# Kernel optimization log

Hardware: AMD Instinct MI355X
Metric: run time of the kernel (lower is better)

The kernel has to match this reference:

```python
import jax, jax.numpy as jnp
import numpy as np

BS, N_STK, N_STK_PNT = 4, 32, 128
N_PNT = N_STK * N_STK_PNT
SP_IN, DN_IN = 128, 128
SP_OUT, DN_OUT = 256, 256
SP_NEAR, DN_NEAR = 2, 10
COOR = 128


def _conv2d(x, w, b, stride=(1, 1), pad='VALID'):
    # x [bs,C,H,W], w [O,I,kh,kw]
    y = jax.lax.conv_general_dilated(x, w, window_strides=stride, padding=pad,
                                     dimension_numbers=('NCHW', 'OIHW', 'NCHW'))
    return y + b[None, :, None, None]


def _fps(xyz, n_sample):
    # farthest point sampling. xyz [bs,n,c] -> [bs,n_sample] int32
    n = xyz.shape[1]

    def one(x):
        def body(i, state):
            idx, dist, far = state
            idx = idx.at[i].set(far)
            d = jnp.sum((x - x[far]) ** 2, axis=-1)
            dist = jnp.minimum(dist, d)
            return idx, dist, jnp.argmax(dist).astype(jnp.int32)

        idx0 = jnp.zeros((n_sample,), jnp.int32)
        dist0 = jnp.full((n,), 1e10, x.dtype)
        idx, _, _ = jax.lax.fori_loop(0, n_sample, body, (idx0, dist0, jnp.int32(0)))
        return idx

    return jax.vmap(one)(xyz)


def _gcn(x, W, b, g, bt, k):
    # DGCNN edge-conv. x [bs,c,n]; W [2c,co]
    xt = jnp.swapaxes(x, 1, 2)                                   # [bs,n,c]
    sq = jnp.sum(xt * xt, axis=-1)                               # [bs,n]
    dist = sq[:, :, None] - 2.0 * jnp.einsum('bnc,bmc->bnm', xt, xt) + sq[:, None, :]
    _, idx = jax.lax.top_k(-dist, k)                             # [bs,n,k]
    nbr = jax.vmap(lambda p, i: p[i])(xt, idx)                   # [bs,n,k,c]
    ctr = jnp.broadcast_to(xt[:, :, None, :], nbr.shape)
    edge = jnp.concatenate([ctr, nbr - ctr], axis=-1)            # [bs,n,k,2c]
    h = jnp.einsum('bnke,eo->bnko', edge, W) + b
    h = jax.nn.relu(g * h + bt)
    return jnp.swapaxes(jnp.max(h, axis=2), 1, 2)                # [bs,co,n]


def setup_inputs() -> dict:
    key = jax.random.key(0)
    ks = jax.random.split(key, 16)
    f32 = jnp.float32
    d = {
        'sparse_fea': jax.random.normal(ks[0], (BS, SP_IN, N_STK), f32),
        'dense_fea': jax.random.normal(ks[1], (BS, DN_IN, N_PNT), f32),
        'stk_coor': jax.random.normal(ks[2], (BS, N_STK, COOR), f32),
        # DenseToSparse: Conv2d(dn_in->dn_in, (1,3)) + BN
        'd2s_w': jax.random.normal(ks[3], (DN_IN, DN_IN, 1, 3), f32) * 0.05,
        'd2s_b': jnp.zeros((DN_IN,), f32),
        'd2s_g': jnp.ones((DN_IN,), f32),
        'd2s_bt': jnp.zeros((DN_IN,), f32),
        # sparse GCN: in = SP_IN + DN_IN, edge feat 2*in
        'sp_W': jax.random.normal(ks[4], (2 * (SP_IN + DN_IN), SP_OUT), f32) * 0.05,
        'sp_b': jnp.zeros((SP_OUT,), f32),
        'sp_g': jnp.ones((SP_OUT,), f32),
        'sp_bt': jnp.zeros((SP_OUT,), f32),
        # dense GCN: in = DN_IN + SP_IN
        'dn_W': jax.random.normal(ks[5], (2 * (DN_IN + SP_IN), DN_OUT), f32) * 0.05,
        'dn_b': jnp.zeros((DN_OUT,), f32),
        'dn_g': jnp.ones((DN_OUT,), f32),
        'dn_bt': jnp.zeros((DN_OUT,), f32),
        # DownSample: Conv2d(dn_out->dn_out, (1,3), stride (1,2), pad (0,1)) + BN
        'ds_w': jax.random.normal(ks[6], (DN_OUT, DN_OUT, 1, 3), f32) * 0.05,
        'ds_b': jnp.zeros((DN_OUT,), f32),
        'ds_g': jnp.ones((DN_OUT,), f32),
        'ds_bt': jnp.zeros((DN_OUT,), f32),
    }
    return d


def reference(sparse_fea, dense_fea, stk_coor,
              d2s_w, d2s_b, d2s_g, d2s_bt,
              sp_W, sp_b, sp_g, sp_bt,
              dn_W, dn_b, dn_g, dn_bt,
              ds_w, ds_b, ds_g, ds_bt):
    bs = sparse_fea.shape[0]
    df = dense_fea.reshape(bs, DN_IN, N_STK, N_STK_PNT)
    # DenseToSparse: conv (1,3) valid + BN(eval) + relu + max over stroke points
    h = _conv2d(df, d2s_w, d2s_b)
    h = jax.nn.relu(d2s_g[None, :, None, None] * h + d2s_bt[None, :, None, None])
    sp_from_dn = jnp.max(h, axis=3)                                    # [bs,dn_in,n_stk]
    union_sparse = jnp.concatenate([sparse_fea, sp_from_dn], axis=1)   # [bs,sp_in+dn_in,n_stk]
    # SparseToDense: broadcast stroke feature onto its points
    dn_from_sp = jnp.broadcast_to(sparse_fea[:, :, :, None], (bs, SP_IN, N_STK, N_STK_PNT))
    union_dense = jnp.concatenate([df, dn_from_sp], axis=1).reshape(bs, DN_IN + SP_IN, N_PNT)
    # GCN (DGCNN edge conv) updates
    sparse_up = _gcn(union_sparse, sp_W, sp_b, sp_g, sp_bt, SP_NEAR)   # [bs,SP_OUT,n_stk]
    dense_up = _gcn(union_dense, dn_W, dn_b, dn_g, dn_bt, DN_NEAR)     # [bs,DN_OUT,n_pnt]
    # DownSample: FPS on stroke coords, gather strokes, strided conv on points
    n_half = N_STK // 2
    fps_idx = _fps(stk_coor, n_half)                                   # [bs,n_half]
    stk_coor_s = jnp.take_along_axis(stk_coor, fps_idx[:, :, None], axis=1)
    sp_s = jnp.take_along_axis(jnp.swapaxes(sparse_up, 1, 2), fps_idx[:, :, None], axis=1)
    sp_s = jnp.swapaxes(sp_s, 1, 2)                                    # [bs,SP_OUT,n_half]
    dn = dense_up.reshape(bs, DN_OUT, N_STK, N_STK_PNT)
    dn = jnp.take_along_axis(dn, fps_idx[:, None, :, None], axis=2)    # [bs,DN_OUT,n_half,n_stk_pnt]
    dn = _conv2d(dn, ds_w, ds_b, stride=(1, 2), pad=[(0, 0), (1, 1)])
    dn = jax.nn.relu(ds_g[None, :, None, None] * dn + ds_bt[None, :, None, None])
    dn = dn.reshape(bs, DN_OUT, n_half * (N_STK_PNT // 2))
    return sp_s, dn, stk_coor_s
```

## Files before the change

### kernel.cpp

```cpp
#include <hip/hip_runtime.h>

#define NPNT 4096
#define NSTK 32

typedef _Float16 half8 __attribute__((ext_vector_type(8)));
typedef float f32x4 __attribute__((ext_vector_type(4)));
typedef unsigned long long u64;

static const size_t OFF_XT   = 0;
static const size_t OFF_P    = 4194304;
static const size_t OFF_Q    = 8388608;
static const size_t OFF_SQD  = 12582912;
static const size_t OFF_SPFD = 12599296;
static const size_t OFF_XS   = 12615680;
static const size_t OFF_PS   = 12648448;
static const size_t OFF_QS   = 12681216;
static const size_t OFF_WSP  = 12746752;
static const size_t OFF_KNN  = 13402112;
static const size_t OFF_IDXS = 13565952;
static const size_t OFF_FPS  = 13566208;
static const size_t OFF_SD   = 13566272;

__device__ __forceinline__ void insertK(u64 lk[10], u64 k) {
  if (k >= lk[9]) return;
  lk[9] = k;
#pragma unroll
  for (int j = 9; j > 0; j--) {
    u64 a = lk[j-1], b2 = lk[j];
    bool sw = b2 < a;
    lk[j-1] = sw ? b2 : a;
    lk[j]   = sw ? a : b2;
  }
}

#define CASK(a, b) { u64 _x = (a), _y = (b); bool _s = _y < _x; \
  (a) = _s ? _y : _x; (b) = _s ? _x : _y; }

__device__ __forceinline__ void merge10(u64 lk[10], const u64 b[10]) {
  u64 c[10];
#pragma unroll
  for (int i = 0; i < 10; i++) { u64 t = b[9 - i]; u64 a = lk[i]; c[i] = a < t ? a : t; }
  CASK(c[0], c[5]); CASK(c[1], c[6]); CASK(c[2], c[7]); CASK(c[3], c[8]); CASK(c[4], c[9]);
  CASK(c[0], c[1]); CASK(c[1], c[2]); CASK(c[2], c[3]); CASK(c[3], c[4]);
  CASK(c[0], c[1]); CASK(c[1], c[2]); CASK(c[2], c[3]);
  CASK(c[0], c[1]); CASK(c[1], c[2]);
  CASK(c[0], c[1]);
  CASK(c[5], c[6]); CASK(c[6], c[7]); CASK(c[7], c[8]); CASK(c[8], c[9]);
  CASK(c[5], c[6]); CASK(c[6], c[7]); CASK(c[7], c[8]);
  CASK(c[5], c[6]); CASK(c[6], c[7]);
  CASK(c[5], c[6]);
#pragma unroll
  for (int i = 0; i < 10; i++) lk[i] = c[i];
}

__global__ __launch_bounds__(256) void k_pre(
    const float* __restrict__ df, const float* __restrict__ sf,
    const float* __restrict__ coor, const float* __restrict__ dnW,
    const float* __restrict__ d2sw, const float* __restrict__ d2scb,
    const float* __restrict__ d2sg, const float* __restrict__ d2sbt,
    const float* __restrict__ dsw,
    _Float16* __restrict__ XH, _Float16* __restrict__ XL, float* __restrict__ sqd,
    _Float16* __restrict__ WPh, _Float16* __restrict__ WPl,
    _Float16* __restrict__ WQh, _Float16* __restrict__ WQl,
    float* __restrict__ WDP,
    float* __restrict__ spfd, int* __restrict__ fpsidx, float* __restrict__ out2) {
  __shared__ __align__(16) char SMEM[46080];
  const int bid = blockIdx.x;
  const int t = threadIdx.x;

  if (bid < 4) {
    int b = bid;
    float (*X)[132] = (float (*)[132])SMEM;
    float* dist = (float*)(SMEM + 16896);
    int* far_s  = (int*)(SMEM + 17024);
    int* sel    = (int*)(SMEM + 17028);
    for (int idx = t; idx < 32 * 32; idx += 256) {
      int r = idx >> 5, q = idx & 31;
      *(float4*)&X[r][q * 4] = *(const float4*)&coor[((size_t)b * 32 + r) * 128 + q * 4];
    }
    if (t < 32) dist[t] = 1e10f;
    if (t == 0) *far_s = 0;
    __syncthreads();
    for (int it = 0; it < 16; it++) {
      int far = *far_s;
      if (t == 0) sel[it] = far;
      if (t < 32) {
        float d = 0.0f;
        for (int c = 0; c < 128; c++) { float dd = X[t][c] - X[far][c]; d = fmaf(dd, dd, d); }
        float dm = dist[t];
        dist[t] = d < dm ? d : dm;
      }
      __syncthreads();
      if (t == 0) {
        float best = -1.0f; int bi = 0;
        for (int m = 0; m < 32; m++) if (dist[m] > best) { best = dist[m]; bi = m; }
        *far_s = bi;
      }
      __syncthreads();
    }
    if (t < 16) fpsidx[b * 16 + t] = sel[t];
    __syncthreads();
    for (int idx = t; idx < 16 * 32; idx += 256) {
      int j = idx >> 5, q = idx & 31;
      *(float4*)&out2[((size_t)b * 16 + j) * 128 + q * 4] = *(const float4*)&X[sel[j]][q * 4];
    }
  } else if (bid < 260) {
    int idx0 = bid - 4;
    int b = idx0 & 3, n0 = (idx0 >> 2) * 64;
    int s0 = n0 >> 7;
    float (*T)[68] = (float (*)[68])SMEM;
    _Float16* Sh = (_Float16*)(SMEM + 34816);
    _Float16* Sl = (_Float16*)(SMEM + 35072);
    {
      int c = t >> 1, nh = (t & 1) * 32;
      const float* src = &df[((size_t)b * 128 + c) * NPNT + n0 + nh];
#pragma unroll
      for (int j = 0; j < 8; j++) *(float4*)&T[c][nh + j * 4] = *(const float4*)&src[j * 4];
    }
    if (t < 128) {
      float x = sf[((size_t)b * 128 + t) * NSTK + s0];
      _Float16 hi = (_Float16)x;
      Sh[t] = hi; Sl[t] = (_Float16)(x - (float)hi);
    }
    __syncthreads();
    {
      int n = t >> 2, cseg = (t & 3) * 32;
      size_t base = ((size_t)b * NPNT + n0 + n) * 256;
      float s = 0.0f;
#pragma unroll
      for (int k = 0; k < 4; k++) {
        half8 hv, lv, shv, slv;
#pragma unroll
        for (int e = 0; e < 8; e++) {
          float x = T[cseg + k * 8 + e][n];
          s = fmaf(x, x, s);
          _Float16 hi = (_Float16)x;
          hv[e] = hi; lv[e] = (_Float16)(x - (float)hi);
          shv[e] = Sh[cseg + k * 8 + e];
          slv[e] = Sl[cseg + k * 8 + e];
        }
        *(half8*)&XH[base + cseg + k * 8] = hv;
        *(half8*)&XL[base + cseg + k * 8] = lv;
        *(half8*)&XH[base + 128 + cseg + k * 8] = shv;
        *(half8*)&XL[base + 128 + cseg + k * 8] = slv;
      }
      s += __shfl_xor(s, 1);
      s += __shfl_xor(s, 2);
      if ((t & 3) == 0) sqd[(size_t)b * NPNT + n0 + n] = s;
    }
  } else if (bid < 516) {
    int idx0 = bid - 260;
    int b = idx0 & 3, o0 = ((idx0 >> 2) & 1) * 64, s = idx0 >> 3;
    int n0 = s * 128;
    float (*A)[64]   = (float (*)[64])SMEM;
    float (*Bs)[132] = (float (*)[132])(SMEM + 24576);
    float (*Dr)[17]  = (float (*)[17])(SMEM + 41472);
    float acc[4][8];
#pragma unroll
    for (int i = 0; i < 4; i++)
#pragma unroll
      for (int j = 0; j < 8; j++) acc[i][j] = 0.0f;
    int tn = t & 15, to = t >> 4;
    for (int ic = 0; ic < 128; ic += 32) {
      {
        int ol = t >> 2, q = t & 3;
        const float* src = &d2sw[((size_t)(o0 + ol) * 128 + ic) * 3 + q * 24];
#pragma unroll
        for (int r = 0; r < 6; r++) {
          float4 v = *(const float4*)&src[r * 4];
          int e = q * 24 + r * 4;
          A[e+0][ol] = v.x; A[e+1][ol] = v.y; A[e+2][ol] = v.z; A[e+3][ol] = v.w;
        }
      }
      for (int idx = t; idx < 32 * 33; idx += 256) {
        int row = idx / 33, f4 = idx % 33;
        int nb = n0 + f4 * 4;
        const float* srow = &df[((size_t)b * 128 + ic + row) * NPNT];
        float4 v;
        if (nb + 3 < NPNT) v = *(const float4*)&srow[nb];
        else {
          v.x = srow[nb   < NPNT ? nb   : NPNT-1];
          v.y = srow[nb+1 < NPNT ? nb+1 : NPNT-1];
          v.z = srow[nb+2 < NPNT ? nb+2 : NPNT-1];
          v.w = srow[nb+3 < NPNT ? nb+3 : NPNT-1];
// ... 15 lines not shown
            float bvj = bv[kw + j];
            acc[0][j] = fmaf(av.x, bvj, acc[0][j]);
            acc[1][j] = fmaf(av.y, bvj, acc[1][j]);
            acc[2][j] = fmaf(av.z, bvj, acc[2][j]);
            acc[3][j] = fmaf(av.w, bvj, acc[3][j]);
          }
        }
      }
      __syncthreads();
    }
#pragma unroll
    for (int i = 0; i < 4; i++) {
      int o = o0 + to * 4 + i;
      float gg = d2sg[o], bb = d2scb[o], bo = d2sbt[o];
      float m = 0.0f;
#pragma unroll
      for (int j = 0; j < 8; j++) {
        int p = tn * 8 + j;
        if (p < 126) {
          float v = fmaf(gg, acc[i][j] + bb, bo);
          v = v > 0.0f ? v : 0.0f;
          m = v > m ? v : m;
        }
      }
      Dr[to * 4 + i][tn] = m;
    }
    __syncthreads();
    if (t < 64) {
      float m = 0.0f;
#pragma unroll
      for (int k = 0; k < 16; k++) m = Dr[t][k] > m ? Dr[t][k] : m;
      spfd[((size_t)b * 128 + o0 + t) * NSTK + s] = m;
    }
  } else if (bid < 772) {
    int k = bid - 516, o = t;
    float w1 = dnW[(size_t)k * 256 + o];
    float w2 = dnW[(size_t)(k + 256) * 256 + o];
    float p = w1 - w2;
    _Float16 ph = (_Float16)p;  WPh[(size_t)o * 256 + k] = ph;
    WPl[(size_t)o * 256 + k] = (_Float16)(p - (float)ph);
    _Float16 qh = (_Float16)w2; WQh[(size_t)o * 256 + k] = qh;
    WQl[(size_t)o * 256 + k] = (_Float16)(w2 - (float)qh);
  } else {
    int o = bid - 772;
    const float* src = &dsw[(size_t)o * 768];
    float* dst = &WDP[(size_t)o * 768];
#pragma unroll
    for (int kw = 0; kw < 3; kw++)
      dst[kw * 256 + t] = src[t * 3 + kw];
  }
}

__global__ __launch_bounds__(256) void k_sparse_graph(const float* __restrict__ sf, const float* __restrict__ spfd,
    float* __restrict__ xs, int* __restrict__ idxs, float* __restrict__ SD) {
  int b = blockIdx.x, t = threadIdx.x;
  __shared__ float X[32][260];
  __shared__ float sq[32];
  __shared__ float D[32][33];
  for (int idx = t; idx < 32 * 256; idx += 256) {
    int n = idx >> 8, c = idx & 255;
    float v = (c < 128) ? sf[((size_t)b * 128 + c) * NSTK + n]
                        : spfd[((size_t)b * 128 + (c - 128)) * NSTK + n];
    X[n][c] = v;
  }
  __syncthreads();
  for (int idx = t; idx < 32 * 64; idx += 256) {
    int n = idx >> 6, q = idx & 63;
    *(float4*)&xs[((size_t)b * 32 + n) * 256 + q * 4] = *(const float4*)&X[n][q * 4];
  }
#pragma unroll
  for (int rep = 0; rep < 4; rep++) {
    int p = t + rep * 256;
    int s = p >> 5, u = p & 31;
    float acc = 0.0f;
    for (int c = 0; c < 128; c++) {
      float d = X[s][c] - X[u][c];
      acc = fmaf(d, d, acc);
    }
    SD[(size_t)b * 1024 + p] = acc;
  }
  if (t < 32) {
    float s = 0.0f;
    for (int c = 0; c < 256; c++) s = fmaf(X[t][c], X[t][c], s);
    sq[t] = s;
  }
  __syncthreads();
  {
    int n = t >> 3;
    for (int mg = 0; mg < 4; mg++) {
      int m = (t & 7) + mg * 8;
      float dot = 0.0f;
      for (int c = 0; c < 256; c++) dot = fmaf(X[n][c], X[m][c], dot);
      D[n][m] = (sq[n] - 2.0f * dot) + sq[m];
    }
  }
  __syncthreads();
  if (t < 32) {
    float d0 = 1e30f, d1 = 1e30f; int i0 = 0, i1 = 0;
    for (int m = 0; m < 32; m++) {
      float d = D[t][m];
      if (d < d0) { d1 = d0; i1 = i0; d0 = d; i0 = m; }
      else if (d < d1) { d1 = d; i1 = m; }
    }
    idxs[(b * 32 + t) * 2 + 0] = i0;
    idxs[(b * 32 + t) * 2 + 1] = i1;
  }
}

__global__ __launch_bounds__(256) void k_sparse_pq(const float* __restrict__ xs, const float* __restrict__ W,
    float* __restrict__ Ps, float* __restrict__ Qs) {
  int b = blockIdx.x >> 5, n = blockIdx.x & 31;
  int o = threadIdx.x;
  const float* xr = &xs[((size_t)b * 32 + n) * 256];
  float accP = 0.0f, accQ = 0.0f;
  for (int c = 0; c < 256; c++) {
    float xc = xr[c];
    float w1 = W[(size_t)c * 256 + o];
    float w2 = W[(size_t)(c + 256) * 256 + o];
    accP = fmaf(xc, w1 - w2, accP);
    accQ = fmaf(xc, w2, accQ);
  }
  Ps[((size_t)b * 32 + n) * 256 + o] = accP;
  Qs[((size_t)b * 32 + n) * 256 + o] = accQ;
}

__global__ __launch_bounds__(256) void k_sparse_cg(const float* __restrict__ Ps, const float* __restrict__ Qs,
    const int* __restrict__ idxs, const int* __restrict__ fps,
    const float* __restrict__ g, const float* __restrict__ cb, const float* __restrict__ bt,
    float* __restrict__ out0) {
  int b = blockIdx.x, j = blockIdx.y, o = threadIdx.x;
  int n = fps[b * 16 + j];
  int i0 = idxs[(b * 32 + n) * 2 + 0], i1 = idxs[(b * 32 + n) * 2 + 1];
  float p = Ps[((size_t)b * 32 + n) * 256 + o];
  float q0 = Qs[((size_t)b * 32 + i0) * 256 + o];
  float q1 = Qs[((size_t)b * 32 + i1) * 256 + o];
  float gg = g[o], bb = cb[o], bo = bt[o];
  float h0 = fmaf(gg, p + q0 + bb, bo); h0 = h0 > 0.0f ? h0 : 0.0f;
  float h1 = fmaf(gg, p + q1 + bb, bo); h1 = h1 > 0.0f ? h1 : 0.0f;
  out0[((size_t)b * 256 + o) * 16 + j] = h0 > h1 ? h0 : h1;
}

#define STAGE(ch2_, p_) { \
  int srow = t >> 2, scol = (t & 3) * 16; \
  size_t gp = (bofs + (size_t)(m0 + (ch2_) * 64 + srow)) * 256 + (p_) * 64 + scol; \
  float4 gh0 = *(const float4*)&XH[gp]; float4 gh1 = *(const float4*)&XH[gp + 8]; \
  float4 gl0 = *(const float4*)&XL[gp]; float4 gl1 = *(const float4*)&XL[gp + 8]; \
  int lo = srow * 72 + scol; \
  *(float4*)&BshH[lo] = gh0; *(float4*)&BshH[lo + 8] = gh1; \
  *(float4*)&BshL[lo] = gl0; *(float4*)&BshL[lo + 8] = gl1; }

#define DWU(wv_, r_, c_) DwU[(((wv_) * 16 + (r_)) * 68) + (c_)]

__global__ __launch_bounds__(256, 4) void k_knn_mfma(const _Float16* __restrict__ XH,
    const _Float16* __restrict__ XL, const float* __restrict__ sqd, const float* __restrict__ SD,
    const int* __restrict__ fps, u64* __restrict__ pk) {
  const int h = blockIdx.x, rb = blockIdx.y, b = blockIdx.z;
  const int t = threadIdx.x;
  const int w = t >> 6, L = t & 63;
  const int c15 = L & 15, q = L >> 4;
  const int jst = rb >> 1;
  const int ph = (rb & 1) * 64;
  const int s_stk = fps[b * 16 + jst];
  const int nsrc = s_stk * 128 + ph + w * 16;
  const int rc0 = rb * 64 + w * 16;
  const size_t bofs = (size_t)b * NPNT;

  __shared__ __align__(16) char SMEM[18432];
  _Float16* const BshH = (_Float16*)SMEM;
  _Float16* const BshL = (_Float16*)(SMEM + 64 * 72 * 2);
  unsigned* const DwU = (unsigned*)SMEM;

  half8 ah[4], al[4];
  {
    const _Float16* ap  = XH + (bofs + nsrc + c15) * 256 + q * 8;
    const _Float16* apl = XL + (bofs + nsrc + c15) * 256 + q * 8;
#pragma unroll
    for (int ch = 0; ch < 4; ch++) {
      ah[ch] = *(const half8*)(ap + ch * 32);
      al[ch] = *(const half8*)(apl + ch * 32);
    }
  }
  float snr[4];
#pragma unroll
  for (int r = 0; r < 4; r++) snr[r] = sqd[bofs + nsrc + q * 4 + r];

  u64 lk[10];
#pragma unroll
  for (int j = 0; j < 10; j++) lk[j] = ~0ull;
// ... 54 lines not shown

#pragma unroll
      for (int cg = 0; cg < 4; cg++) {
        float basec = SDv + smv[cg];
#pragma unroll
        for (int r = 0; r < 4; r++) {
          float d = fmaf(-2.0f, acc[cg][r], snr[r] + basec);
          unsigned uu = __float_as_uint(d);
          unsigned kk = uu ^ ((unsigned)((int)uu >> 31) | 0x80000000u);
          DWU(w, q * 4 + r, cg * 16 + c15) = kk;
        }
      }
#pragma unroll
      for (int jj = 0; jj < 4; jj++) {
        uint4 kv = *(const uint4*)&DWU(w, r_sel, jj * 16 + sl * 4);
        int ib = m0 + ch2 * 64 + jj * 16 + sl * 4;
        insertK(lk, ((u64)kv.x << 32) | (unsigned)(ib + 0));
        insertK(lk, ((u64)kv.y << 32) | (unsigned)(ib + 1));
        insertK(lk, ((u64)kv.z << 32) | (unsigned)(ib + 2));
        insertK(lk, ((u64)kv.w << 32) | (unsigned)(ib + 3));
      }
    }
  }

#pragma unroll
  for (int m = 1; m <= 2; m <<= 1) {
    u64 o[10];
#pragma unroll
    for (int j = 0; j < 10; j++) o[j] = __shfl_xor(lk[j], m);
    merge10(lk, o);
  }
  if (sl == 0) {
    size_t row = (size_t)b * 2048 + rc0 + r_sel;
    u64* dst = &pk[(row * 16 + h) * 10];
#pragma unroll
    for (int j = 0; j < 10; j++) dst[j] = lk[j];
  }
}

__global__ __launch_bounds__(256) void k_knn_merge(const u64* __restrict__ pk,
                                                   int* __restrict__ knnc) {
  int gid = blockIdx.x * 256 + threadIdx.x;
  size_t row = (size_t)(gid >> 2);
  int sl = gid & 3;
  const u64* src = &pk[row * 160 + (size_t)sl * 40];
  u64 lk[10];
#pragma unroll
  for (int j = 0; j < 10; j++) lk[j] = src[j];
#pragma unroll
  for (int l = 1; l < 4; l++) {
    u64 bv[10];
#pragma unroll
    for (int j = 0; j < 10; j++) bv[j] = src[l * 10 + j];
    merge10(lk, bv);
  }
#pragma unroll
  for (int m = 1; m <= 2; m <<= 1) {
    u64 o[10];
#pragma unroll
    for (int j = 0; j < 10; j++) o[j] = __shfl_xor(lk[j], m);
    merge10(lk, o);
  }
  if (sl == 0) {
#pragma unroll
    for (int j = 0; j < 10; j++) knnc[row * 10 + j] = (int)(unsigned)(lk[j] & 0xffffffffull);
  }
}

__global__ __launch_bounds__(256, 4) void k_pq_mfma(const _Float16* __restrict__ XH, const _Float16* __restrict__ XL,
    const _Float16* __restrict__ WPh, const _Float16* __restrict__ WPl,
    const _Float16* __restrict__ WQh, const _Float16* __restrict__ WQl,
    const int* __restrict__ fps, const float* __restrict__ g, const float* __restrict__ cb,
    const float* __restrict__ bt, float* __restrict__ Pc, float* __restrict__ Qp) {
  const int b = blockIdx.z;
  const int t = threadIdx.x, w = t >> 6, L = t & 63;
  const int c15 = L & 15, q = L >> 4;
  const int ow = blockIdx.y * 128 + (w >> 1) * 64;
  const size_t bofs = (size_t)b * NPNT;
  f32x4 zz = {0.0f, 0.0f, 0.0f, 0.0f};

  {
    const int nw = blockIdx.x * 32 + (w & 1) * 16;
    f32x4 accQ[4];
#pragma unroll
    for (int cg = 0; cg < 4; cg++) accQ[cg] = zz;
    const _Float16* ap  = XH + (bofs + nw + c15) * 256 + q * 8;
    const _Float16* apl = XL + (bofs + nw + c15) * 256 + q * 8;
#pragma unroll
    for (int ch = 0; ch < 8; ch++) {
      half8 a_h = *(const half8*)(ap + ch * 32);
      half8 a_l = *(const half8*)(apl + ch * 32);
#pragma unroll
      for (int cg = 0; cg < 4; cg++) {
        size_t wb = (size_t)(ow + cg * 16 + c15) * 256 + ch * 32 + q * 8;
        half8 bqh = *(const half8*)(WQh + wb);
        half8 bql = *(const half8*)(WQl + wb);
        accQ[cg] = __builtin_amdgcn_mfma_f32_16x16x32_f16(a_h, bqh, accQ[cg], 0, 0, 0);
        accQ[cg] = __builtin_amdgcn_mfma_f32_16x16x32_f16(a_h, bql, accQ[cg], 0, 0, 0);
        accQ[cg] = __builtin_amdgcn_mfma_f32_16x16x32_f16(a_l, bqh, accQ[cg], 0, 0, 0);
      }
    }
#pragma unroll
// ... 11 lines not shown
    const int m0 = blockIdx.x * 32 + (w & 1) * 16;
    const int jst = m0 >> 7;
    const int pbase = m0 & 127;
    const int nsrc = fps[b * 16 + jst] * 128 + pbase;
    f32x4 accP[4];
#pragma unroll
    for (int cg = 0; cg < 4; cg++) accP[cg] = zz;
    const _Float16* ap  = XH + (bofs + nsrc + c15) * 256 + q * 8;
    const _Float16* apl = XL + (bofs + nsrc + c15) * 256 + q * 8;
#pragma unroll
    for (int ch = 0; ch < 8; ch++) {
      half8 a_h = *(const half8*)(ap + ch * 32);
      half8 a_l = *(const half8*)(apl + ch * 32);
#pragma unroll
      for (int cg = 0; cg < 4; cg++) {
        size_t wb = (size_t)(ow + cg * 16 + c15) * 256 + ch * 32 + q * 8;
        half8 bph = *(const half8*)(WPh + wb);
        half8 bpl = *(const half8*)(WPl + wb);
        accP[cg] = __builtin_amdgcn_mfma_f32_16x16x32_f16(a_h, bph, accP[cg], 0, 0, 0);
        accP[cg] = __builtin_amdgcn_mfma_f32_16x16x32_f16(a_h, bpl, accP[cg], 0, 0, 0);
        accP[cg] = __builtin_amdgcn_mfma_f32_16x16x32_f16(a_l, bph, accP[cg], 0, 0, 0);
      }
    }
#pragma unroll
    for (int cg = 0; cg < 4; cg++) {
      int o = ow + cg * 16 + c15;
      float gg = g[o], bb = cb[o], bo = bt[o];
#pragma unroll
      for (int r = 0; r < 4; r++) {
        Pc[(((size_t)b * 16 + jst) * 128 + pbase + q * 4 + r) * 256 + o] =
            fmaf(gg, accP[cg][r] + bb, bo);
      }
    }
  }
}

__global__ __launch_bounds__(256) void k_build_M(const float* __restrict__ Pc, const float* __restrict__ Qp,
    const int* __restrict__ knnc, float* __restrict__ M) {
  int pc = blockIdx.x, j = blockIdx.y, b = blockIdx.z;
  int t = threadIdx.x;
  int p0 = pc * 16;
#pragma unroll 1
  for (int pi = 0; pi < 16; pi++) {
    size_t m = ((size_t)b * 16 + j) * 128 + p0 + pi;
    float pv = Pc[m * 256 + t];
    const int* id = &knnc[m * 10];
    float mx = 0.0f;
#pragma unroll
    for (int k = 0; k < 10; k++) {
      float qv = Qp[((size_t)b * NPNT + id[k]) * 256 + t];
      float h = pv + qv;
      mx = h > mx ? h : mx;
    }
    M[m * 256 + t] = mx;
  }
}

__global__ __launch_bounds__(256) void k_ds_gemm(const float* __restrict__ WDP, const float* __restrict__ M,
    const float* __restrict__ cb, const float* __restrict__ g, const float* __restrict__ bt,
    float* __restrict__ out1) {
  int j = blockIdx.x, o0 = blockIdx.y * 64, b = blockIdx.z;
  int j0 = j * 64;
  int t = threadIdx.x;
  __shared__ float A[32][68];
  __shared__ float Bs[32][68];
  float acc[4][4];
#pragma unroll
  for (int i = 0; i < 4; i++)
#pragma unroll
    for (int jj = 0; jj < 4; jj++) acc[i][jj] = 0.0f;
  int tj = t & 15, to = t >> 4;
  for (int kc = 0; kc < 768; kc += 32) {
    {
      int ol = t >> 2, q = t & 3;
      const float* src = &WDP[(size_t)(o0 + ol) * 768 + kc + q * 8];
      float4 v0 = *(const float4*)src, v1 = *(const float4*)(src + 4);
      int cc = q * 8;
      A[cc+0][ol] = v0.x; A[cc+1][ol] = v0.y; A[cc+2][ol] = v0.z; A[cc+3][ol] = v0.w;
      A[cc+4][ol] = v1.x; A[cc+5][ol] = v1.y; A[cc+6][ol] = v1.z; A[cc+7][ol] = v1.w;
    }
    {
      int jl = t >> 2, q = t & 3;
      int kw = kc >> 8, cbl = (kc & 255) + q * 8;
      int p = 2 * jl - 1 + kw;
      float4 v0, v1;
      if (p >= 0) {
        const float* src = &M[(((size_t)b * 16 + j) * 128 + p) * 256 + cbl];
// ... 32 lines not shown
    *(float4*)&out1[((size_t)b * 256 + o) * 1024 + j0 + tj * 4] = v;
  }
}

extern "C" void kernel_launch(void* const* d_in, const int* in_sizes, int n_in,
                              void* d_out, int out_size, void* d_ws, size_t ws_size,
                              hipStream_t stream) {
  (void)in_sizes; (void)n_in; (void)out_size; (void)ws_size;
  const float* sf    = (const float*)d_in[0];
  const float* df    = (const float*)d_in[1];
  const float* coor  = (const float*)d_in[2];
  const float* d2sw  = (const float*)d_in[3];
  const float* d2sb  = (const float*)d_in[4];
  const float* d2sg  = (const float*)d_in[5];
  const float* d2sbt = (const float*)d_in[6];
  const float* spW   = (const float*)d_in[7];
  const float* spb   = (const float*)d_in[8];
  const float* spg   = (const float*)d_in[9];
  const float* spbt  = (const float*)d_in[10];
  const float* dnW   = (const float*)d_in[11];
  const float* dnb   = (const float*)d_in[12];
  const float* dng   = (const float*)d_in[13];
  const float* dnbt  = (const float*)d_in[14];
  const float* dsw   = (const float*)d_in[15];
  const float* dsb   = (const float*)d_in[16];
  const float* dsg   = (const float*)d_in[17];
  const float* dsbt  = (const float*)d_in[18];

  float* ws   = (float*)d_ws;
  float* Pc   = ws + OFF_P;
  float* Qp   = ws + OFF_Q;
  float* SQD  = ws + OFF_SQD;
  float* SPFD = ws + OFF_SPFD;
  float* XS   = ws + OFF_XS;
  float* PS   = ws + OFF_PS;
  float* QS   = ws + OFF_QS;
  int*   KNNC = (int*)(ws + OFF_KNN);
  int*   IDXS = (int*)(ws + OFF_IDXS);
  int*   FPS  = (int*)(ws + OFF_FPS);
  float* SD   = ws + OFF_SD;
  _Float16* XT2H = (_Float16*)(ws + OFF_XT);
  _Float16* XT2L = XT2H + (size_t)4 * NPNT * 256;
  float* Mb = ws + OFF_XT;
  _Float16* WPh = (_Float16*)(ws + OFF_WSP);
  _Float16* WPl = WPh + 65536;
  _Float16* WQh = WPh + 131072;
  _Float16* WQl = WPh + 196608;
  float* WDP = ws + OFF_WSP + 131072;
  u64* PK = (u64*)(ws + OFF_Q);

  float* out0 = (float*)d_out;
  float* out1 = out0 + 16384;
  float* out2 = out1 + 1048576;

  k_pre<<<dim3(1028), 256, 0, stream>>>(df, sf, coor, dnW, d2sw, d2sb, d2sg, d2sbt, dsw,
                                        XT2H, XT2L, SQD, WPh, WPl, WQh, WQl, WDP,
                                        SPFD, FPS, out2);
  k_sparse_graph<<<dim3(4), 256, 0, stream>>>(sf, SPFD, XS, IDXS, SD);
  k_sparse_pq<<<dim3(128), 256, 0, stream>>>(XS, spW, PS, QS);
  k_sparse_cg<<<dim3(4, 16), 256, 0, stream>>>(PS, QS, IDXS, FPS, spg, spb, spbt, out0);
  k_knn_mfma<<<dim3(16, 32, 4), 256, 0, stream>>>(XT2H, XT2L, SQD, SD, FPS, PK);
  k_knn_merge<<<dim3(128), 256, 0, stream>>>(PK, KNNC);
  k_pq_mfma<<<dim3(128, 2, 4), 256, 0, stream>>>(XT2H, XT2L, WPh, WPl, WQh, WQl,
                                                 FPS, dng, dnb, dnbt, Pc, Qp);
  k_build_M<<<dim3(8, 16, 4), 256, 0, stream>>>(Pc, Qp, KNNC, Mb);
  k_ds_gemm<<<dim3(16, 4, 4), 256, 0, stream>>>(WDP, Mb, dsb, dsg, dsbt, out1);
}
```

Baseline: 417.2 us.

## Fuse sparse GCN kernels, merge kNN reduction into build_M, compact candidate storage

The three sparse-branch kernels become one single-block-per-batch kernel that computes neighbours, the Q projection into shared memory and P only for the FPS-selected strokes. The stroke distance matrix SD moves into extra k_pre blocks. The separate kNN merge kernel is removed: k_knn_mfma writes candidates as split 32-bit keys and 16-bit indices, and k_build_M merges the 16 partial lists with shuffles before gathering. Launch order and k_pq_mfma occupancy bounds also change. This cuts launches and intermediate global traffic, but the sparse kernel runs on only 4 blocks and does its GEMMs serially.

```diff
diff --git a/kernel.cpp b/kernel.cpp
--- a/kernel.cpp
+++ b/kernel.cpp
@@ -6,18 +6,15 @@
 typedef _Float16 half8 __attribute__((ext_vector_type(8)));
 typedef float f32x4 __attribute__((ext_vector_type(4)));
 typedef unsigned long long u64;
+typedef unsigned int u32;
+typedef unsigned short u16;
 
 static const size_t OFF_XT   = 0;
 static const size_t OFF_P    = 4194304;
 static const size_t OFF_Q    = 8388608;
 static const size_t OFF_SQD  = 12582912;
 static const size_t OFF_SPFD = 12599296;
-static const size_t OFF_XS   = 12615680;
-static const size_t OFF_PS   = 12648448;
-static const size_t OFF_QS   = 12681216;
 static const size_t OFF_WSP  = 12746752;
-static const size_t OFF_KNN  = 13402112;
-static const size_t OFF_IDXS = 13565952;
 static const size_t OFF_FPS  = 13566208;
 static const size_t OFF_SD   = 13566272;
 
@@ -62,7 +59,7 @@
     _Float16* __restrict__ XH, _Float16* __restrict__ XL, float* __restrict__ sqd,
     _Float16* __restrict__ WPh, _Float16* __restrict__ WPl,
     _Float16* __restrict__ WQh, _Float16* __restrict__ WQl,
-    float* __restrict__ WDP,
+    float* __restrict__ WDP, float* __restrict__ SD,
     float* __restrict__ spfd, int* __restrict__ fpsidx, float* __restrict__ out2) {
   __shared__ __align__(16) char SMEM[46080];
   const int bid = blockIdx.x;
@@ -104,8 +101,25 @@
       int j = idx >> 5, q = idx & 31;
       *(float4*)&out2[((size_t)b * 16 + j) * 128 + q * 4] = *(const float4*)&X[sel[j]][q * 4];
     }
-  } else if (bid < 260) {
-    int idx0 = bid - 4;
+  } else if (bid < 8) {
+    int b = bid - 4;
+    float* Xs = (float*)SMEM;
+    for (int k = t; k < 1024; k += 256)
+      *(float4*)&Xs[k * 4] = *(const float4*)&sf[(size_t)b * 4096 + k * 4];
+    __syncthreads();
+#pragma unroll
+    for (int rep = 0; rep < 4; rep++) {
+      int p = t + rep * 256;
+      int s = p >> 5, u = p & 31;
+      float acc = 0.0f;
+      for (int c = 0; c < 128; c++) {
+        float d = Xs[c * 32 + s] - Xs[c * 32 + u];
+        acc = fmaf(d, d, acc);
+      }
+      SD[(size_t)b * 1024 + p] = acc;
+    }
+  } else if (bid < 264) {
+    int idx0 = bid - 8;
     int b = idx0 & 3, n0 = (idx0 >> 2) * 64;
     int s0 = n0 >> 7;
     float (*T)[68] = (float (*)[68])SMEM;
@@ -148,8 +162,8 @@
       s += __shfl_xor(s, 2);
       if ((t & 3) == 0) sqd[(size_t)b * NPNT + n0 + n] = s;
     }
-  } else if (bid < 516) {
-    int idx0 = bid - 260;
+  } else if (bid < 520) {
+    int idx0 = bid - 264;
     int b = idx0 & 3, o0 = ((idx0 >> 2) & 1) * 64, s = idx0 >> 3;
     int n0 = s * 128;
     float (*A)[64]   = (float (*)[64])SMEM;
@@ -231,8 +245,8 @@
       for (int k = 0; k < 16; k++) m = Dr[t][k] > m ? Dr[t][k] : m;
       spfd[((size_t)b * 128 + o0 + t) * NSTK + s] = m;
     }
-  } else if (bid < 772) {
-    int k = bid - 516, o = t;
+  } else if (bid < 776) {
+    int k = bid - 520, o = t;
     float w1 = dnW[(size_t)k * 256 + o];
     float w2 = dnW[(size_t)(k + 256) * 256 + o];
     float p = w1 - w2;
@@ -241,7 +255,7 @@
     _Float16 qh = (_Float16)w2; WQh[(size_t)o * 256 + k] = qh;
     WQl[(size_t)o * 256 + k] = (_Float16)(w2 - (float)qh);
   } else {
-    int o = bid - 772;
+    int o = bid - 776;
     const float* src = &dsw[(size_t)o * 768];
     float* dst = &WDP[(size_t)o * 768];
 #pragma unroll
@@ -250,34 +264,25 @@
   }
 }
 
-__global__ __launch_bounds__(256) void k_sparse_graph(const float* __restrict__ sf, const float* __restrict__ spfd,
-    float* __restrict__ xs, int* __restrict__ idxs, float* __restrict__ SD) {
+__global__ __launch_bounds__(256) void k_sparse_mono(const float* __restrict__ sf,
+    const float* __restrict__ spfd, const int* __restrict__ fps, const float* __restrict__ W,
+    const float* __restrict__ g, const float* __restrict__ cb, const float* __restrict__ bt,
+    float* __restrict__ out0) {
   int b = blockIdx.x, t = threadIdx.x;
   __shared__ float X[32][260];
+  __shared__ float Qs[32][256];
+  __shared__ float D[32][33];
   __shared__ float sq[32];
-  __shared__ float D[32][33];
+  __shared__ int idxs_s[64];
+  __shared__ int fps_s[16];
   for (int idx = t; idx < 32 * 256; idx += 256) {
     int n = idx >> 8, c = idx & 255;
     float v = (c < 128) ? sf[((size_t)b * 128 + c) * NSTK + n]
                         : spfd[((size_t)b * 128 + (c - 128)) * NSTK + n];
     X[n][c] = v;
   }
+  if (t < 16) fps_s[t] = fps[b * 16 + t];
   __syncthreads();
-  for (int idx = t; idx < 32 * 64; idx += 256) {
-    int n = idx >> 6, q = idx & 63;
-    *(float4*)&xs[((size_t)b * 32 + n) * 256 + q * 4] = *(const float4*)&X[n][q * 4];
-  }
-#pragma unroll
-  for (int rep = 0; rep < 4; rep++) {
-    int p = t + rep * 256;
-    int s = p >> 5, u = p & 31;
-    float acc = 0.0f;
-    for (int c = 0; c < 128; c++) {
-      float d = X[s][c] - X[u][c];
-      acc = fmaf(d, d, acc);
-    }
-    SD[(size_t)b * 1024 + p] = acc;
-  }
   if (t < 32) {
     float s = 0.0f;
     for (int c = 0; c < 256; c++) s = fmaf(X[t][c], X[t][c], s);
@@ -301,42 +306,75 @@
       if (d < d0) { d1 = d0; i1 = i0; d0 = d; i0 = m; }
       else if (d < d1) { d1 = d; i1 = m; }
     }
-    idxs[(b * 32 + t) * 2 + 0] = i0;
-    idxs[(b * 32 + t) * 2 + 1] = i1;
-  }
-}
-
-__global__ __launch_bounds__(256) void k_sparse_pq(const float* __restrict__ xs, const float* __restrict__ W,
-    float* __restrict__ Ps, float* __restrict__ Qs) {
-  int b = blockIdx.x >> 5, n = blockIdx.x & 31;
-  int o = threadIdx.x;
-  const float* xr = &xs[((size_t)b * 32 + n) * 256];
-  float accP = 0.0f, accQ = 0.0f;
-  for (int c = 0; c < 256; c++) {
-    float xc = xr[c];
-    float w1 = W[(size_t)c * 256 + o];
-    float w2 = W[(size_t)(c + 256) * 256 + o];
-    accP = fmaf(xc, w1 - w2, accP);
-    accQ = fmaf(xc, w2, accQ);
-  }
-  Ps[((size_t)b * 32 + n) * 256 + o] = accP;
-  Qs[((size_t)b * 32 + n) * 256 + o] = accQ;
-}
-
-__global__ __launch_bounds__(256) void k_sparse_cg(const float* __restrict__ Ps, const float* __restrict__ Qs,
-    const int* __restrict__ idxs, const int* __restrict__ fps,
-    const float* __restrict__ g, const float* __restrict__ cb, const float* __restrict__ bt,
-    float* __restrict__ out0) {
-  int b = blockIdx.x, j = blockIdx.y, o = threadIdx.x;
-  int n = fps[b * 16 + j];
-  int i0 = idxs[(b * 32 + n) * 2 + 0], i1 = idxs[(b * 32 + n) * 2 + 1];
-  float p = Ps[((size_t)b * 32 + n) * 256 + o];
-  float q0 = Qs[((size_t)b * 32 + i0) * 256 + o];
-  float q1 = Qs[((size_t)b * 32 + i1) * 256 + o];
+    idxs_s[t * 2 + 0] = i0;
+    idxs_s[t * 2 + 1] = i1;
+  }
+  const int o = t;
+#pragma unroll 1
+  for (int nc = 0; nc < 4; nc++) {
+    float acc[8];
+#pragma unroll
+    for (int nn = 0; nn < 8; nn++) acc[nn] = 0.0f;
+    for (int c4 = 0; c4 < 64; c4++) {
+      float4 xv[8];
+#pragma unroll
+      for (int nn = 0; nn < 8; nn++) xv[nn] = *(const float4*)&X[nc * 8 + nn][c4 * 4];
+      int c = c4 * 4;
+      float w0 = W[(size_t)(c + 256) * 256 + o];
+      float w1 = W[(size_t)(c + 257) * 256 + o];
+      float w2 = W[(size_t)(c + 258) * 256 + o];
+      float w3 = W[(size_t)(c + 259) * 256 + o];
+#pragma unroll
+      for (int nn = 0; nn < 8; nn++) {
+        acc[nn] = fmaf(xv[nn].x, w0, acc[nn]);
+        acc[nn] = fmaf(xv[nn].y, w1, acc[nn]);
+        acc[nn] = fmaf(xv[nn].z, w2, acc[nn]);
+        acc[nn] = fmaf(xv[nn].w, w3, acc[nn]);
+      }
+    }
+#pragma unroll
+    for (int nn = 0; nn < 8; nn++) Qs[nc * 8 + nn][o] = acc[nn];
+  }
+  float pacc[16];
+#pragma unroll 1
+  for (int jc = 0; jc < 2; jc++) {
+    int fs[8];
+#pragma unroll
+    for (int jj = 0; jj < 8; jj++) fs[jj] = fps_s[jc * 8 + jj];
+    float acc[8];
+#pragma unroll
+    for (int jj = 0; jj < 8; jj++) acc[jj] = 0.0f;
+    for (int c4 = 0; c4 < 64; c4++) {
+      float4 xv[8];
+#pragma unroll
+      for (int jj = 0; jj < 8; jj++) xv[jj] = *(const float4*)&X[fs[jj]][c4 * 4];
+      int c = c4 * 4;
+      float p0 = W[(size_t)(c + 0) * 256 + o] - W[(size_t)(c + 256) * 256 + o];
+      float p1 = W[(size_t)(c + 1) * 256 + o] - W[(size_t)(c + 257) * 256 + o];
+      float p2 = W[(size_t)(c + 2) * 256 + o] - W[(size_t)(c + 258) * 256 + o];
+      float p3 = W[(size_t)(c + 3) * 256 + o] - W[(size_t)(c + 259) * 256 + o];
+#pragma unroll
+      for (int jj = 0; jj < 8; jj++) {
+        acc[jj] = fmaf(xv[jj].x, p0, acc[jj]);
+        acc[jj] = fmaf(xv[jj].y, p1, acc[jj]);
+        acc[jj] = fmaf(xv[jj].z, p2, acc[jj]);
+        acc[jj] = fmaf(xv[jj].w, p3, acc[jj]);
+      }
+    }
+#pragma unroll
+    for (int jj = 0; jj < 8; jj++) pacc[jc * 8 + jj] = acc[jj];
+  }
+  __syncthreads();
   float gg = g[o], bb = cb[o], bo = bt[o];
-  float h0 = fmaf(gg, p + q0 + bb, bo); h0 = h0 > 0.0f ? h0 : 0.0f;
-  float h1 = fmaf(gg, p + q1 + bb, bo); h1 = h1 > 0.0f ? h1 : 0.0f;
-  out0[((size_t)b * 256 + o) * 16 + j] = h0 > h1 ? h0 : h1;
+#pragma unroll
+  for (int j = 0; j < 16; j++) {
+    int n = fps_s[j];
+    int i0 = idxs_s[n * 2 + 0], i1 = idxs_s[n * 2 + 1];
+    float p = pacc[j];
+    float h0 = fmaf(gg, p + Qs[i0][o] + bb, bo); h0 = h0 > 0.0f ? h0 : 0.0f;
+    float h1 = fmaf(gg, p + Qs[i1][o] + bb, bo); h1 = h1 > 0.0f ? h1 : 0.0f;
+    out0[((size_t)b * 256 + o) * 16 + j] = h0 > h1 ? h0 : h1;
+  }
 }
 
 #define STAGE(ch2_, p_) { \
@@ -352,7 +390,7 @@
 
 __global__ __launch_bounds__(256, 4) void k_knn_mfma(const _Float16* __restrict__ XH,
     const _Float16* __restrict__ XL, const float* __restrict__ sqd, const float* __restrict__ SD,
-    const int* __restrict__ fps, u64* __restrict__ pk) {
+    const int* __restrict__ fps, u32* __restrict__ pkd, u16* __restrict__ pki) {
   const int h = blockIdx.x, rb = blockIdx.y, b = blockIdx.z;
   const int t = threadIdx.x;
   const int w = t >> 6, L = t & 63;
@@ -473,42 +511,58 @@
   }
   if (sl == 0) {
     size_t row = (size_t)b * 2048 + rc0 + r_sel;
-    u64* dst = &pk[(row * 16 + h) * 10];
-#pragma unroll
-    for (int j = 0; j < 10; j++) dst[j] = lk[j];
-  }
-}
-
-__global__ __launch_bounds__(256) void k_knn_merge(const u64* __restrict__ pk,
-                                                   int* __restrict__ knnc) {
-  int gid = blockIdx.x * 256 + threadIdx.x;
-  size_t row = (size_t)(gid >> 2);
-  int sl = gid & 3;
-  const u64* src = &pk[row * 160 + (size_t)sl * 40];
-  u64 lk[10];
-#pragma unroll
-  for (int j = 0; j < 10; j++) lk[j] = src[j];
-#pragma unroll
-  for (int l = 1; l < 4; l++) {
-    u64 bv[10];
-#pragma unroll
-    for (int j = 0; j < 10; j++) bv[j] = src[l * 10 + j];
-    merge10(lk, bv);
-  }
-#pragma unroll
-  for (int m = 1; m <= 2; m <<= 1) {
-    u64 o[10];
-#pragma unroll
-    for (int j = 0; j < 10; j++) o[j] = __shfl_xor(lk[j], m);
-    merge10(lk, o);
-  }
-  if (sl == 0) {
-#pragma unroll
-    for (int j = 0; j < 10; j++) knnc[row * 10 + j] = (int)(unsigned)(lk[j] & 0xffffffffull);
-  }
-}
-
-__global__ __launch_bounds__(256, 4) void k_pq_mfma(const _Float16* __restrict__ XH, const _Float16* __restrict__ XL,
+    u32* dk = &pkd[(row * 16 + h) * 10];
+    u16* di = &pki[(row * 16 + h) * 10];
+#pragma unroll
+    for (int j = 0; j < 10; j++) {
+      dk[j] = (u32)(lk[j] >> 32);
+      di[j] = (u16)(lk[j] & 0xffffull);
+    }
+  }
+}
+
+__global__ __launch_bounds__(256) void k_build_M(const float* __restrict__ Pc, const float* __restrict__ Qp,
+    const u32* __restrict__ pkd, const u16* __restrict__ pki, float* __restrict__ M) {
+  int pc = blockIdx.x, j = blockIdx.y, b = blockIdx.z;
+  int t = threadIdx.x;
+  __shared__ int knn_s[16][10];
+  {
+    int rr = t >> 4, ll = t & 15;
+    size_t row = (size_t)b * 2048 + j * 128 + pc * 16 + rr;
+    const u32* kd = &pkd[(row * 16 + ll) * 10];
+    const u16* ki = &pki[(row * 16 + ll) * 10];
+    u64 lk[10];
+#pragma unroll
+    for (int jj = 0; jj < 10; jj++) lk[jj] = ((u64)kd[jj] << 32) | (u64)ki[jj];
+#pragma unroll
+    for (int m = 1; m <= 8; m <<= 1) {
+      u64 o[10];
+#pragma unroll
+      for (int jj = 0; jj < 10; jj++) o[jj] = __shfl_xor(lk[jj], m);
+      merge10(lk, o);
+    }
+    if (ll == 0) {
+#pragma unroll
+      for (int jj = 0; jj < 10; jj++) knn_s[rr][jj] = (int)(lk[jj] & 0xffffull);
+    }
+  }
+  __syncthreads();
+#pragma unroll 1
+  for (int pi = 0; pi < 16; pi++) {
+    size_t m = ((size_t)b * 16 + j) * 128 + pc * 16 + pi;
+    float pv = Pc[m * 256 + t];
+    float mx = 0.0f;
+#pragma unroll
+    for (int k = 0; k < 10; k++) {
+      float qv = Qp[((size_t)b * NPNT + knn_s[pi][k]) * 256 + t];
+      float h = pv + qv;
+      mx = h > mx ? h : mx;
+    }
+    M[m * 256 + t] = mx;
+  }
+}
+
+__global__ __launch_bounds__(256, 2) void k_pq_mfma(const _Float16* __restrict__ XH, const _Float16* __restrict__ XL,
     const _Float16* __restrict__ WPh, const _Float16* __restrict__ WPl,
     const _Float16* __restrict__ WQh, const _Float16* __restrict__ WQl,
     const int* __restrict__ fps, const float* __restrict__ g, const float* __restrict__ cb,
@@ -586,27 +640,6 @@
             fmaf(gg, accP[cg][r] + bb, bo);
       }
     }
-  }
-}
-
-__global__ __launch_bounds__(256) void k_build_M(const float* __restrict__ Pc, const float* __restrict__ Qp,
-    const int* __restrict__ knnc, float* __restrict__ M) {
-  int pc = blockIdx.x, j = blockIdx.y, b = blockIdx.z;
-  int t = threadIdx.x;
-  int p0 = pc * 16;
-#pragma unroll 1
-  for (int pi = 0; pi < 16; pi++) {
-    size_t m = ((size_t)b * 16 + j) * 128 + p0 + pi;
-    float pv = Pc[m * 256 + t];
-    const int* id = &knnc[m * 10];
-    float mx = 0.0f;
-#pragma unroll
-    for (int k = 0; k < 10; k++) {
-      float qv = Qp[((size_t)b * NPNT + id[k]) * 256 + t];
-      float h = pv + qv;
-      mx = h > mx ? h : mx;
-    }
-    M[m * 256 + t] = mx;
   }
 }
 
@@ -705,11 +738,6 @@
   float* Qp   = ws + OFF_Q;
   float* SQD  = ws + OFF_SQD;
   float* SPFD = ws + OFF_SPFD;
-  float* XS   = ws + OFF_XS;
-  float* PS   = ws + OFF_PS;
-  float* QS   = ws + OFF_QS;
-  int*   KNNC = (int*)(ws + OFF_KNN);
-  int*   IDXS = (int*)(ws + OFF_IDXS);
   int*   FPS  = (int*)(ws + OFF_FPS);
   float* SD   = ws + OFF_SD;
   _Float16* XT2H = (_Float16*)(ws + OFF_XT);
@@ -720,22 +748,20 @@
   _Float16* WQh = WPh + 131072;
   _Float16* WQl = WPh + 196608;
   float* WDP = ws + OFF_WSP + 131072;
-  u64* PK = (u64*)(ws + OFF_Q);
+  u32* PKD = (u32*)(ws + OFF_P + 2097152);
+  u16* PKI = (u16*)(ws + OFF_P + 2097152 + 1310720);
 
   float* out0 = (float*)d_out;
   float* out1 = out0 + 16384;
   float* out2 = out1 + 1048576;
 
-  k_pre<<<dim3(1028), 256, 0, stream>>>(df, sf, coor, dnW, d2sw, d2sb, d2sg, d2sbt, dsw,
-                                        XT2H, XT2L, SQD, WPh, WPl, WQh, WQl, WDP,
+  k_pre<<<dim3(1032), 256, 0, stream>>>(df, sf, coor, dnW, d2sw, d2sb, d2sg, d2sbt, dsw,
+                                        XT2H, XT2L, SQD, WPh, WPl, WQh, WQl, WDP, SD,
                                         SPFD, FPS, out2);
-  k_sparse_graph<<<dim3(4), 256, 0, stream>>>(sf, SPFD, XS, IDXS, SD);
-  k_sparse_pq<<<dim3(128), 256, 0, stream>>>(XS, spW, PS, QS);
-  k_sparse_cg<<<dim3(4, 16), 256, 0, stream>>>(PS, QS, IDXS, FPS, spg, spb, spbt, out0);
-  k_knn_mfma<<<dim3(16, 32, 4), 256, 0, stream>>>(XT2H, XT2L, SQD, SD, FPS, PK);
-  k_knn_merge<<<dim3(128), 256, 0, stream>>>(PK, KNNC);
+  k_sparse_mono<<<dim3(4), 256, 0, stream>>>(sf, SPFD, FPS, spW, spg, spb, spbt, out0);
   k_pq_mfma<<<dim3(128, 2, 4), 256, 0, stream>>>(XT2H, XT2L, WPh, WPl, WQh, WQl,
                                                  FPS, dng, dnb, dnbt, Pc, Qp);
-  k_build_M<<<dim3(8, 16, 4), 256, 0, stream>>>(Pc, Qp, KNNC, Mb);
+  k_knn_mfma<<<dim3(16, 32, 4), 256, 0, stream>>>(XT2H, XT2L, SQD, SD, FPS, PKD, PKI);
+  k_build_M<<<dim3(8, 16, 4), 256, 0, stream>>>(Pc, Qp, PKD, PKI, Mb);
   k_ds_gemm<<<dim3(16, 4, 4), 256, 0, stream>>>(WDP, Mb, dsb, dsg, dsbt, out1);
 }
```

Measured after the change: 455.1 us. +9.1%, slower.

## Fuse kNN merge into build_M, split packed keys, move stroke distances into prep

Applied to the files above, without the earlier changes.

Removes the separate kNN merge kernel. The partial top-10 lists are now reduced with wave shuffles at the start of the neighbour-max kernel, and the resulting indices are held in shared memory. Partial results are stored as separate 32-bit distance keys and 16-bit indices instead of 64-bit packed words, which cuts the bytes written and read. Stroke-to-stroke distances move from the sparse graph kernel into the prep kernel, the pq GEMM is launched before kNN, and its launch bounds are relaxed. Indices are truncated to 16 bits, which only holds for point indices below 65536, and the merge work is now repeated by every block.

```diff
diff --git a/kernel.cpp b/kernel.cpp
--- a/kernel.cpp
+++ b/kernel.cpp
@@ -6,6 +6,8 @@
 typedef _Float16 half8 __attribute__((ext_vector_type(8)));
 typedef float f32x4 __attribute__((ext_vector_type(4)));
 typedef unsigned long long u64;
+typedef unsigned int u32;
+typedef unsigned short u16;
 
 static const size_t OFF_XT   = 0;
 static const size_t OFF_P    = 4194304;
@@ -16,7 +18,6 @@
 static const size_t OFF_PS   = 12648448;
 static const size_t OFF_QS   = 12681216;
 static const size_t OFF_WSP  = 12746752;
-static const size_t OFF_KNN  = 13402112;
 static const size_t OFF_IDXS = 13565952;
 static const size_t OFF_FPS  = 13566208;
 static const size_t OFF_SD   = 13566272;
@@ -62,7 +63,7 @@
     _Float16* __restrict__ XH, _Float16* __restrict__ XL, float* __restrict__ sqd,
     _Float16* __restrict__ WPh, _Float16* __restrict__ WPl,
     _Float16* __restrict__ WQh, _Float16* __restrict__ WQl,
-    float* __restrict__ WDP,
+    float* __restrict__ WDP, float* __restrict__ SD,
     float* __restrict__ spfd, int* __restrict__ fpsidx, float* __restrict__ out2) {
   __shared__ __align__(16) char SMEM[46080];
   const int bid = blockIdx.x;
@@ -104,8 +105,25 @@
       int j = idx >> 5, q = idx & 31;
       *(float4*)&out2[((size_t)b * 16 + j) * 128 + q * 4] = *(const float4*)&X[sel[j]][q * 4];
     }
-  } else if (bid < 260) {
-    int idx0 = bid - 4;
+  } else if (bid < 8) {
+    int b = bid - 4;
+    float* Xs = (float*)SMEM;
+    for (int k = t; k < 1024; k += 256)
+      *(float4*)&Xs[k * 4] = *(const float4*)&sf[(size_t)b * 4096 + k * 4];
+    __syncthreads();
+#pragma unroll
+    for (int rep = 0; rep < 4; rep++) {
+      int p = t + rep * 256;
+      int s = p >> 5, u = p & 31;
+      float acc = 0.0f;
+      for (int c = 0; c < 128; c++) {
+        float d = Xs[c * 32 + s] - Xs[c * 32 + u];
+        acc = fmaf(d, d, acc);
+      }
+      SD[(size_t)b * 1024 + p] = acc;
+    }
+  } else if (bid < 264) {
+    int idx0 = bid - 8;
     int b = idx0 & 3, n0 = (idx0 >> 2) * 64;
     int s0 = n0 >> 7;
     float (*T)[68] = (float (*)[68])SMEM;
@@ -148,8 +166,8 @@
       s += __shfl_xor(s, 2);
       if ((t & 3) == 0) sqd[(size_t)b * NPNT + n0 + n] = s;
     }
-  } else if (bid < 516) {
-    int idx0 = bid - 260;
+  } else if (bid < 520) {
+    int idx0 = bid - 264;
     int b = idx0 & 3, o0 = ((idx0 >> 2) & 1) * 64, s = idx0 >> 3;
     int n0 = s * 128;
     float (*A)[64]   = (float (*)[64])SMEM;
@@ -231,8 +249,8 @@
       for (int k = 0; k < 16; k++) m = Dr[t][k] > m ? Dr[t][k] : m;
       spfd[((size_t)b * 128 + o0 + t) * NSTK + s] = m;
     }
-  } else if (bid < 772) {
-    int k = bid - 516, o = t;
+  } else if (bid < 776) {
+    int k = bid - 520, o = t;
     float w1 = dnW[(size_t)k * 256 + o];
     float w2 = dnW[(size_t)(k + 256) * 256 + o];
     float p = w1 - w2;
@@ -241,7 +259,7 @@
     _Float16 qh = (_Float16)w2; WQh[(size_t)o * 256 + k] = qh;
     WQl[(size_t)o * 256 + k] = (_Float16)(w2 - (float)qh);
   } else {
-    int o = bid - 772;
+    int o = bid - 776;
     const float* src = &dsw[(size_t)o * 768];
     float* dst = &WDP[(size_t)o * 768];
 #pragma unroll
@@ -251,7 +269,7 @@
 }
 
 __global__ __launch_bounds__(256) void k_sparse_graph(const float* __restrict__ sf, const float* __restrict__ spfd,
-    float* __restrict__ xs, int* __restrict__ idxs, float* __restrict__ SD) {
+    float* __restrict__ xs, int* __restrict__ idxs) {
   int b = blockIdx.x, t = threadIdx.x;
   __shared__ float X[32][260];
   __shared__ float sq[32];
@@ -266,17 +284,6 @@
   for (int idx = t; idx < 32 * 64; idx += 256) {
     int n = idx >> 6, q = idx & 63;
     *(float4*)&xs[((size_t)b * 32 + n) * 256 + q * 4] = *(const float4*)&X[n][q * 4];
-  }
-#pragma unroll
-  for (int rep = 0; rep < 4; rep++) {
-    int p = t + rep * 256;
-    int s = p >> 5, u = p & 31;
-    float acc = 0.0f;
-    for (int c = 0; c < 128; c++) {
-      float d = X[s][c] - X[u][c];
-      acc = fmaf(d, d, acc);
-    }
-    SD[(size_t)b * 1024 + p] = acc;
   }
   if (t < 32) {
     float s = 0.0f;
@@ -352,7 +359,7 @@
 
 __global__ __launch_bounds__(256, 4) void k_knn_mfma(const _Float16* __restrict__ XH,
     const _Float16* __restrict__ XL, const float* __restrict__ sqd, const float* __restrict__ SD,
-    const int* __restrict__ fps, u64* __restrict__ pk) {
+    const int* __restrict__ fps, u32* __restrict__ pkd, u16* __restrict__ pki) {
   const int h = blockIdx.x, rb = blockIdx.y, b = blockIdx.z;
   const int t = threadIdx.x;
   const int w = t >> 6, L = t & 63;
@@ -473,42 +480,58 @@
   }
   if (sl == 0) {
     size_t row = (size_t)b * 2048 + rc0 + r_sel;
-    u64* dst = &pk[(row * 16 + h) * 10];
-#pragma unroll
-    for (int j = 0; j < 10; j++) dst[j] = lk[j];
-  }
-}
-
-__global__ __launch_bounds__(256) void k_knn_merge(const u64* __restrict__ pk,
-                                                   int* __restrict__ knnc) {
-  int gid = blockIdx.x * 256 + threadIdx.x;
-  size_t row = (size_t)(gid >> 2);
-  int sl = gid & 3;
-  const u64* src = &pk[row * 160 + (size_t)sl * 40];
-  u64 lk[10];
-#pragma unroll
-  for (int j = 0; j < 10; j++) lk[j] = src[j];
-#pragma unroll
-  for (int l = 1; l < 4; l++) {
-    u64 bv[10];
-#pragma unroll
-    for (int j = 0; j < 10; j++) bv[j] = src[l * 10 + j];
-    merge10(lk, bv);
-  }
-#pragma unroll
-  for (int m = 1; m <= 2; m <<= 1) {
-    u64 o[10];
-#pragma unroll
-    for (int j = 0; j < 10; j++) o[j] = __shfl_xor(lk[j], m);
-    merge10(lk, o);
-  }
-  if (sl == 0) {
-#pragma unroll
-    for (int j = 0; j < 10; j++) knnc[row * 10 + j] = (int)(unsigned)(lk[j] & 0xffffffffull);
-  }
-}
-
-__global__ __launch_bounds__(256, 4) void k_pq_mfma(const _Float16* __restrict__ XH, const _Float16* __restrict__ XL,
+    u32* dk = &pkd[(row * 16 + h) * 10];
+    u16* di = &pki[(row * 16 + h) * 10];
+#pragma unroll
+    for (int j = 0; j < 10; j++) {
+      dk[j] = (u32)(lk[j] >> 32);
+      di[j] = (u16)(lk[j] & 0xffffull);
+    }
+  }
+}
+
+__global__ __launch_bounds__(256) void k_build_M(const float* __restrict__ Pc, const float* __restrict__ Qp,
+    const u32* __restrict__ pkd, const u16* __restrict__ pki, float* __restrict__ M) {
+  int pc = blockIdx.x, j = blockIdx.y, b = blockIdx.z;
+  int t = threadIdx.x;
+  __shared__ int knn_s[16][10];
+  {
+    int rr = t >> 4, ll = t & 15;
+    size_t row = (size_t)b * 2048 + j * 128 + pc * 16 + rr;
+    const u32* kd = &pkd[(row * 16 + ll) * 10];
+    const u16* ki = &pki[(row * 16 + ll) * 10];
+    u64 lk[10];
+#pragma unroll
+    for (int jj = 0; jj < 10; jj++) lk[jj] = ((u64)kd[jj] << 32) | (u64)ki[jj];
+#pragma unroll
+    for (int m = 1; m <= 8; m <<= 1) {
+      u64 o[10];
+#pragma unroll
+      for (int jj = 0; jj < 10; jj++) o[jj] = __shfl_xor(lk[jj], m);
+      merge10(lk, o);
+    }
+    if (ll == 0) {
+#pragma unroll
+      for (int jj = 0; jj < 10; jj++) knn_s[rr][jj] = (int)(lk[jj] & 0xffffull);
+    }
+  }
+  __syncthreads();
+#pragma unroll 1
+  for (int pi = 0; pi < 16; pi++) {
+    size_t m = ((size_t)b * 16 + j) * 128 + pc * 16 + pi;
+    float pv = Pc[m * 256 + t];
+    float mx = 0.0f;
+#pragma unroll
+    for (int k = 0; k < 10; k++) {
+      float qv = Qp[((size_t)b * NPNT + knn_s[pi][k]) * 256 + t];
+      float h = pv + qv;
+      mx = h > mx ? h : mx;
+    }
+    M[m * 256 + t] = mx;
+  }
+}
+
+__global__ __launch_bounds__(256, 2) void k_pq_mfma(const _Float16* __restrict__ XH, const _Float16* __restrict__ XL,
     const _Float16* __restrict__ WPh, const _Float16* __restrict__ WPl,
     const _Float16* __restrict__ WQh, const _Float16* __restrict__ WQl,
     const int* __restrict__ fps, const float* __restrict__ g, const float* __restrict__ cb,
@@ -586,27 +609,6 @@
             fmaf(gg, accP[cg][r] + bb, bo);
       }
     }
-  }
-}
-
-__global__ __launch_bounds__(256) void k_build_M(const float* __restrict__ Pc, const float* __restrict__ Qp,
-    const int* __restrict__ knnc, float* __restrict__ M) {
-  int pc = blockIdx.x, j = blockIdx.y, b = blockIdx.z;
-  int t = threadIdx.x;
-  int p0 = pc * 16;
-#pragma unroll 1
-  for (int pi = 0; pi < 16; pi++) {
-    size_t m = ((size_t)b * 16 + j) * 128 + p0 + pi;
-    float pv = Pc[m * 256 + t];
-    const int* id = &knnc[m * 10];
-    float mx = 0.0f;
-#pragma unroll
-    for (int k = 0; k < 10; k++) {
-      float qv = Qp[((size_t)b * NPNT + id[k]) * 256 + t];
-      float h = pv + qv;
-      mx = h > mx ? h : mx;
-    }
-    M[m * 256 + t] = mx;
   }
 }
 
@@ -708,7 +710,6 @@
   float* XS   = ws + OFF_XS;
   float* PS   = ws + OFF_PS;
   float* QS   = ws + OFF_QS;
-  int*   KNNC = (int*)(ws + OFF_KNN);
   int*   IDXS = (int*)(ws + OFF_IDXS);
   int*   FPS  = (int*)(ws + OFF_FPS);
   float* SD   = ws + OFF_SD;
@@ -720,22 +721,22 @@
   _Float16* WQh = WPh + 131072;
   _Float16* WQl = WPh + 196608;
   float* WDP = ws + OFF_WSP + 131072;
-  u64* PK = (u64*)(ws + OFF_Q);
+  u32* PKD = (u32*)(ws + OFF_P + 2097152);
+  u16* PKI = (u16*)(ws + OFF_P + 2097152 + 1310720);
 
   float* out0 = (float*)d_out;
   float* out1 = out0 + 16384;
   float* out2 = out1 + 1048576;
 
-  k_pre<<<dim3(1028), 256, 0, stream>>>(df, sf, coor, dnW, d2sw, d2sb, d2sg, d2sbt, dsw,
-                                        XT2H, XT2L, SQD, WPh, WPl, WQh, WQl, WDP,
+  k_pre<<<dim3(1032), 256, 0, stream>>>(df, sf, coor, dnW, d2sw, d2sb, d2sg, d2sbt, dsw,
+                                        XT2H, XT2L, SQD, WPh, WPl, WQh, WQl, WDP, SD,
                                         SPFD, FPS, out2);
-  k_sparse_graph<<<dim3(4), 256, 0, stream>>>(sf, SPFD, XS, IDXS, SD);
+  k_sparse_graph<<<dim3(4), 256, 0, stream>>>(sf, SPFD, XS, IDXS);
   k_sparse_pq<<<dim3(128), 256, 0, stream>>>(XS, spW, PS, QS);
   k_sparse_cg<<<dim3(4, 16), 256, 0, stream>>>(PS, QS, IDXS, FPS, spg, spb, spbt, out0);
-  k_knn_mfma<<<dim3(16, 32, 4), 256, 0, stream>>>(XT2H, XT2L, SQD, SD, FPS, PK);
-  k_knn_merge<<<dim3(128), 256, 0, stream>>>(PK, KNNC);
   k_pq_mfma<<<dim3(128, 2, 4), 256, 0, stream>>>(XT2H, XT2L, WPh, WPl, WQh, WQl,
                                                  FPS, dng, dnb, dnbt, Pc, Qp);
-  k_build_M<<<dim3(8, 16, 4), 256, 0, stream>>>(Pc, Qp, KNNC, Mb);
+  k_knn_mfma<<<dim3(16, 32, 4), 256, 0, stream>>>(XT2H, XT2L, SQD, SD, FPS, PKD, PKI);
+  k_build_M<<<dim3(8, 16, 4), 256, 0, stream>>>(Pc, Qp, PKD, PKI, Mb);
   k_ds_gemm<<<dim3(16, 4, 4), 256, 0, stream>>>(WDP, Mb, dsb, dsg, dsbt, out1);
 }
```

Result: faster. 406.0 us (-2.7%).
